# Performance work log

Measured on AMD Instinct MI355X. Metric: run time of the kernel, lower is better.

## Reference

```python
import jax, jax.numpy as jnp
import numpy as np

N_NODES = 50000
N_EDGES = 800000
DIMS = [128, 512, 256, 128]
EPS = 1e-5


def setup_inputs() -> dict:
    key = jax.random.key(0)
    ks = jax.random.split(key, 2 + 5 * 3)
    inp = {
        "x": jax.random.normal(ks[0], (N_NODES, DIMS[0]), dtype=jnp.float32),
        "edge_index": jax.random.randint(ks[1], (2, N_EDGES), 0, N_NODES, dtype=jnp.int64),
    }
    ki = 2
    for i in range(3):
        din, dout = DIMS[i], DIMS[i + 1]
        s = 1.0 / np.sqrt(din)
        inp[f"Wl{i}"] = jax.random.uniform(ks[ki + 0], (din, dout), jnp.float32, -s, s)
        inp[f"bl{i}"] = jax.random.uniform(ks[ki + 1], (dout,), jnp.float32, -s, s)
        inp[f"Wr{i}"] = jax.random.uniform(ks[ki + 2], (din, dout), jnp.float32, -s, s)
        inp[f"g{i}"] = jnp.ones((dout,), jnp.float32)
        inp[f"b{i}"] = jnp.zeros((dout,), jnp.float32)
        ki += 5
    return inp


def _sage_mean(x, src, dst, Wl, bl, Wr):
    n = x.shape[0]
    agg = jax.ops.segment_sum(x[src], dst, num_segments=n)  # [N, din]
    deg = jax.ops.segment_sum(jnp.ones((src.shape[0],), x.dtype), dst, num_segments=n)
    mean = agg / jnp.maximum(deg, 1.0)[:, None]
    return mean @ Wl + bl + x @ Wr


def _bn(h, gamma, beta):
    m = h.mean(axis=0)
    v = h.var(axis=0)
    return gamma * (h - m) * jax.lax.rsqrt(v + EPS) + beta


def reference(x, edge_index, Wl0, bl0, Wr0, g0, b0, Wl1, bl1, Wr1, g1, b1, Wl2, bl2, Wr2, g2, b2):
    src, dst = edge_index[0], edge_index[1]
    params = [(Wl0, bl0, Wr0, g0, b0), (Wl1, bl1, Wr1, g1, b1), (Wl2, bl2, Wr2, g2, b2)]
    h = x
    for Wl, bl, Wr, g, b in params:
        h = _sage_mean(h, src, dst, Wl, bl, Wr)
        h = _bn(h, g, b)
        h = jax.nn.relu(h)
        # dropout: identity in eval mode
    return h
```

## Files before the change

kernel.cpp:

```cpp
#include <hip/hip_runtime.h>
#include <cstdint>
#include <cstddef>


#define EPS_BN 1e-5f

typedef unsigned short ushort_t;
typedef __attribute__((ext_vector_type(8))) short short8;
typedef __attribute__((ext_vector_type(4))) float float4v;

__device__ __forceinline__ float bf2f(ushort_t u) {
    union { unsigned int i; float f; } v; v.i = ((unsigned int)u) << 16; return v.f;
}
__device__ __forceinline__ ushort_t f2bf(float f) {
    union { float f; unsigned int i; } v; v.f = f;
    unsigned int r = v.i + 0x7fffu + ((v.i >> 16) & 1u);
    return (ushort_t)(r >> 16);
}

__device__ __forceinline__ void async_copy16(void* lds, const void* g) {
    __builtin_amdgcn_global_load_lds(
        (const __attribute__((address_space(1))) unsigned int*)g,
        (__attribute__((address_space(3))) unsigned int*)lds, 16, 0, 0);
}

__global__ void detect_fmt_kernel(const int* __restrict__ edges, int* __restrict__ nz) {
    int t = threadIdx.x;
    int cnt = 0;
    #pragma unroll
    for (int j = 0; j < 4; ++j) {
        int idx = 2 * (t * 4 + j) + 1;
        if (edges[idx] != 0) cnt++;
    }
    if (cnt) atomicAdd(nz, cnt);
}

__device__ __forceinline__ void edge_sd(const int* __restrict__ p, int e, int ne,
                                        bool is64, int& s, int& d) {
    if (is64) { s = p[2 * e];  d = p[2 * ne + 2 * e]; }
    else      { s = p[e];      d = p[ne + e]; }
}
__device__ __forceinline__ int edge_d(const int* __restrict__ p, int e, int ne, bool is64) {
    return is64 ? p[2 * ne + 2 * e] : p[ne + e];
}

#define EPB 2048

__global__ __launch_bounds__(256) void bhist_kernel(
    const int* __restrict__ edges, int ne, const int* __restrict__ nz,
    int* __restrict__ gcnt) {
    __shared__ int h[256];
    int t = threadIdx.x;
    h[t] = 0;
    __syncthreads();
    bool is64 = (*nz == 0);
    int base_e = blockIdx.x * EPB;
    #pragma unroll
    for (int u = 0; u < EPB / 256; ++u) {
        int i = base_e + u * 256 + t;
        if (i < ne) atomicAdd(&h[edge_d(edges, i, ne, is64) >> 8], 1);
    }
    __syncthreads();
    if (h[t]) atomicAdd(&gcnt[t], h[t]);
}

__global__ __launch_bounds__(256) void bscan_kernel(
    const int* __restrict__ gcnt, int nb, int ne,
    int* __restrict__ bbase, int* __restrict__ bcur) {
    __shared__ int sh[256];
    int t = threadIdx.x;
    int v = (t < nb) ? gcnt[t] : 0;
    sh[t] = v;
    __syncthreads();
    for (int o = 1; o < 256; o <<= 1) {
        int x = (t >= o) ? sh[t - o] : 0;
        __syncthreads();
        sh[t] += x;
        __syncthreads();
    }
    int excl = sh[t] - v;
    if (t < nb) { bbase[t] = excl; bcur[t] = excl; }
    if (t == nb) bbase[t] = ne;
    if (nb == 256 && t == 0) {  }
    if (t == 0 && nb == 256) bbase[256] = ne;
}

__global__ __launch_bounds__(256) void bscatter_kernel(
    const int* __restrict__ edges, int ne, const int* __restrict__ nz,
    int* __restrict__ bcur, int* __restrict__ packed) {
    __shared__ int h[256];
    __shared__ int chunkb[256];
    __shared__ int lcur[256];
    int t = threadIdx.x;
    h[t] = 0;
    lcur[t] = 0;
    __syncthreads();
    bool is64 = (*nz == 0);
    int base_e = blockIdx.x * EPB;
    int ent[EPB / 256], eb[EPB / 256];
    #pragma unroll
    for (int u = 0; u < EPB / 256; ++u) {
        int i = base_e + u * 256 + t;
        if (i < ne) {
            int s, d;
            edge_sd(edges, i, ne, is64, s, d);
            ent[u] = s | ((d & 255) << 24);
            eb[u] = d >> 8;
            atomicAdd(&h[eb[u]], 1);
        } else eb[u] = -1;
    }
    __syncthreads();
    if (h[t]) chunkb[t] = atomicAdd(&bcur[t], h[t]);
    __syncthreads();
    #pragma unroll
    for (int u = 0; u < EPB / 256; ++u) {
        if (eb[u] >= 0) {
            int lp = atomicAdd(&lcur[eb[u]], 1);
            packed[chunkb[eb[u]] + lp] = ent[u];
        }
    }
}

__global__ __launch_bounds__(256) void bbuild_kernel(
    const int* __restrict__ packed, const int* __restrict__ bbase,
    int* __restrict__ rowptr, int* __restrict__ csr_src, int n) {
    __shared__ int h[256];
    __shared__ int cur[256];
    int t = threadIdx.x;
    int bb = blockIdx.x;
    int base = bbase[bb], cnt = bbase[bb + 1] - base;
    h[t] = 0;
    __syncthreads();
    for (int i = t; i < cnt; i += 256)
        atomicAdd(&h[(unsigned)packed[base + i] >> 24], 1);
    __syncthreads();
    int v = h[t];
    for (int o = 1; o < 256; o <<= 1) {
        int x = (t >= o) ? h[t - o] : 0;
        __syncthreads();
        h[t] += x;
        __syncthreads();
    }
    int excl = h[t] - v;
    int node = bb * 256 + t;
    if (node <= n) rowptr[node] = base + excl;
    cur[t] = excl;
    __syncthreads();
    for (int i = t; i < cnt; i += 256) {
        int e = packed[base + i];
        int lp = atomicAdd(&cur[(unsigned)e >> 24], 1);
        csr_src[base + lp] = e & 0xffffff;
    }
}

__global__ void f2b_kernel(const float* __restrict__ in, ushort_t* __restrict__ out, int n) {
    int i = blockIdx.x * 256 + threadIdx.x;
    if (i < n) out[i] = f2bf(in[i]);
}

__global__ void prep_wt_kernel(const float* __restrict__ Wl, const float* __restrict__ Wr,
                               ushort_t* __restrict__ WT, int K1, int Dout) {
    int idx = blockIdx.x * 256 + threadIdx.x;
    int K2 = 2 * K1;
    if (idx >= Dout * K2) return;
    int n = idx / K2, k = idx - n * K2;
    float v = (k < K1) ? Wl[(size_t)k * Dout + n] : Wr[(size_t)(k - K1) * Dout + n];
    WT[idx] = f2bf(v);
}

__global__ void prep_wtc_kernel(const float* __restrict__ Wl, const float* __restrict__ Wr,
                                ushort_t* __restrict__ WTc, int K, int D) {
    int idx = blockIdx.x * 256 + threadIdx.x;
    if (idx >= 2 * D * K) return;
    int nn = idx / K, k = idx - nn * K;
    float v = (nn < D) ? Wl[(size_t)k * D + nn] : Wr[(size_t)k * D + (nn - D)];
    WTc[idx] = f2bf(v);
}

template <int VEC> struct VecT;
template <> struct VecT<2> { using T = unsigned int; };
template <> struct VecT<4> { using T = uint2; };
template <> struct VecT<8> { using T = uint4; };

template <int VEC>
__device__ __forceinline__ void vunpack(typename VecT<VEC>::T v, unsigned int* w) {
    if constexpr (VEC == 2) { w[0] = v; }
    else if constexpr (VEC == 4) { w[0] = v.x; w[1] = v.y; }
    else { w[0] = v.x; w[1] = v.y; w[2] = v.z; w[3] = v.w; }
}

template <int VEC>
__device__ __forceinline__ void vaccum(typename VecT<VEC>::T v, float* acc) {
    unsigned int w[VEC / 2];
    vunpack<VEC>(v, w);
    #pragma unroll
    for (int i = 0; i < VEC / 2; ++i) {
        acc[2 * i + 0] += bf2f((ushort_t)(w[i] & 0xffffu));
        acc[2 * i + 1] += bf2f((ushort_t)(w[i] >> 16));
    }
}

template <int VEC>
__device__ __forceinline__ void gather_sum(
    const ushort_t* __restrict__ base, const int* __restrict__ csr_src,
    int e0, int e1, int rstride, float* acc) {
    using VT = typename VecT<VEC>::T;
    int e = e0;
    for (; e + 8 <= e1; e += 8) {
        VT v[8];
        #pragma unroll
        for (int u = 0; u < 8; ++u)
            v[u] = *(const VT*)(base + (size_t)csr_src[e + u] * rstride);
        #pragma unroll
        for (int u = 0; u < 8; ++u) vaccum<VEC>(v[u], acc);
    }
    if (e + 4 <= e1) {
        VT v[4];
        #pragma unroll
        for (int u = 0; u < 4; ++u)
            v[u] = *(const VT*)(base + (size_t)csr_src[e + u] * rstride);
        #pragma unroll
        for (int u = 0; u < 4; ++u) vaccum<VEC>(v[u], acc);
        e += 4;
    }
    if (e + 2 <= e1) {
        VT v0 = *(const VT*)(base + (size_t)csr_src[e] * rstride);
        VT v1 = *(const VT*)(base + (size_t)csr_src[e + 1] * rstride);
        vaccum<VEC>(v0, acc); vaccum<VEC>(v1, acc);
        e += 2;
    }
    if (e < e1)
        vaccum<VEC>(*(const VT*)(base + (size_t)csr_src[e] * rstride), acc);
}

template <int VEC>
__global__ __launch_bounds__(256) void aggregate_wave_kernel(
    const ushort_t* __restrict__ h, ushort_t* __restrict__ mean,
    const int* __restrict__ rowptr, const int* __restrict__ csr_src, int nnodes) {
    const int din = VEC * 64;
    int wid = blockIdx.x * 4 + (threadIdx.x >> 6);
    if (wid >= nnodes) return;
    int lane = threadIdx.x & 63;
    int e0 = rowptr[wid], e1 = rowptr[wid + 1];

    float acc[VEC];
    #pragma unroll
    for (int i = 0; i < VEC; ++i) acc[i] = 0.f;
    gather_sum<VEC>(h + (size_t)lane * VEC, csr_src, e0, e1, din, acc);

    int deg = e1 - e0;
    float scale = 1.0f / (float)(deg > 1 ? deg : 1);
    unsigned int o[VEC / 2];
    #pragma unroll
    for (int i = 0; i < VEC / 2; ++i)
        o[i] = (unsigned int)f2bf(acc[2 * i] * scale) |
               ((unsigned int)f2bf(acc[2 * i + 1] * scale) << 16);
    using VT = typename VecT<VEC>::T;
    VT ov;
    if constexpr (VEC == 2) { ov = o[0]; }
    else if constexpr (VEC == 4) { ov.x = o[0]; ov.y = o[1]; }
    else { ov.x = o[0]; ov.y = o[1]; ov.z = o[2]; ov.w = o[3]; }
    *(VT*)(mean + (size_t)wid * din + (size_t)lane * VEC) = ov;
}

template <int VEC>
__global__ __launch_bounds__(256) void aggregate_add_kernel(
    const ushort_t* __restrict__ PR, const float* __restrict__ bias,
    ushort_t* __restrict__ pre,
    const int* __restrict__ rowptr, const int* __restrict__ csr_src, int nnodes) {
    const int D = VEC * 64;
    const int stride = 2 * D;
    int wid = blockIdx.x * 4 + (threadIdx.x >> 6);
    if (wid >= nnodes) return;
    int lane = threadIdx.x & 63;
    int e0 = rowptr[wid], e1 = rowptr[wid + 1];

    float acc[VEC];
    #pragma unroll
    for (int i = 0; i < VEC; ++i) acc[i] = 0.f;
    gather_sum<VEC>(PR + (size_t)lane * VEC, csr_src, e0, e1, stride, acc);

    int deg = e1 - e0;
    float scale = 1.0f / (float)(deg > 1 ? deg : 1);

    using VT = typename VecT<VEC>::T;
    VT rv = *(const VT*)(PR + (size_t)wid * stride + D + (size_t)lane * VEC);
    unsigned int rw[VEC / 2];
    vunpack<VEC>(rv, rw);
    float o[VEC];
    #pragma unroll
    for (int i = 0; i < VEC / 2; ++i) {
        o[2 * i + 0] = bf2f((ushort_t)(rw[i] & 0xffffu));
        o[2 * i + 1] = bf2f((ushort_t)(rw[i] >> 16));
    }
    #pragma unroll
    for (int i = 0; i < VEC; ++i)
        o[i] += acc[i] * scale + bias[lane * VEC + i];

    unsigned int ow[VEC / 2];
    #pragma unroll
    for (int i = 0; i < VEC / 2; ++i)
        ow[i] = (unsigned int)f2bf(o[2 * i]) | ((unsigned int)f2bf(o[2 * i + 1]) << 16);
    VT ov;
    if constexpr (VEC == 2) { ov = ow[0]; }
    else if constexpr (VEC == 4) { ov.x = ow[0]; ov.y = ow[1]; }
    else { ov.x = ow[0]; ov.y = ow[1]; ov.z = ow[2]; ov.w = ow[3]; }
    *(VT*)(pre + (size_t)wid * D + (size_t)lane * VEC) = ov;
}

template <bool DUAL, bool BIAS>
__global__ __launch_bounds__(256) void gemm_glds_kernel(
    const ushort_t* __restrict__ A1, const ushort_t* __restrict__ A2,
    const ushort_t* __restrict__ BT, const float* __restrict__ bias,
    ushort_t* __restrict__ Cb, int N, int K1, int Ktot, int Wtot) {
    __shared__ ushort_t As[128 * 64];
    __shared__ ushort_t Bs[128 * 64];

    const int tid = threadIdx.x;
    const int wave = tid >> 6;
    const int lane = tid & 63;
    const int quad = lane >> 4;
    const int l15 = lane & 15;
    const int sw7 = l15 & 7;
    const int rowBase = blockIdx.y * 128;
    const int colBase = blockIdx.x * 128;
    const int wm = (wave >> 1) * 64;
    const int wn = (wave & 1) * 64;

    float4v acc[4][4];
    #pragma unroll
    for (int i = 0; i < 4; ++i)
        #pragma unroll
        for (int j = 0; j < 4; ++j)
            acc[i][j] = (float4v){0.f, 0.f, 0.f, 0.f};

    const int nkt = Ktot / 64;
    const int khalf = K1 / 64;

    for (int kt = 0; kt < nkt; ++kt) {
        const ushort_t* Asrc = A1;
        int kg = kt * 64;
        if (DUAL && kt >= khalf) { Asrc = A2; kg = (kt - khalf) * 64; }
        const int kb = kt * 64;

        #pragma unroll
        for (int u = 0; u < 4; ++u) {
            int c = u * 256 + tid;
            int r = c >> 3, cc = c & 7;
            int off = (cc ^ (r & 7)) * 8;
            int grow = rowBase + r;
            if (grow >= N) grow = N - 1;
            async_copy16(&As[c * 8], Asrc + (size_t)grow * K1 + kg + off);
            async_copy16(&Bs[c * 8], BT + (size_t)(colBase + r) * Ktot + kb + off);
        }
        __syncthreads();

        #pragma unroll
        for (int kh = 0; kh < 2; ++kh) {
            int cidx = kh * 4 + quad;
            short8 af[4], bf4[4];
            #pragma unroll
            for (int i = 0; i < 4; ++i)
                af[i] = *(const short8*)&As[(wm + i * 16 + l15) * 64 + (cidx ^ sw7) * 8];
            #pragma unroll
            for (int j = 0; j < 4; ++j)
                bf4[j] = *(const short8*)&Bs[(wn + j * 16 + l15) * 64 + (cidx ^ sw7) * 8];
            #pragma unroll
            for (int i = 0; i < 4; ++i)
                #pragma unroll
                for (int j = 0; j < 4; ++j)
                    acc[i][j] = __builtin_amdgcn_mfma_f32_16x16x32_bf16(bf4[j], af[i], acc[i][j], 0, 0, 0);
        }
        __syncthreads();
    }

    ushort_t* lws = &As[wave * 2048];
    #pragma unroll
    for (int p = 0; p < 2; ++p) {
        #pragma unroll
        for (int jj = 0; jj < 2; ++jj) {
            int j = 2 * p + jj;
            float4 bv = make_float4(0.f, 0.f, 0.f, 0.f);
            if (BIAS) bv = *(const float4*)(bias + colBase + wn + j * 16 + quad * 4);
            #pragma unroll
            for (int i = 0; i < 4; ++i) {
                uint2 pk;
                pk.x = (unsigned int)f2bf(acc[i][j][0] + bv.x) |
                       ((unsigned int)f2bf(acc[i][j][1] + bv.y) << 16);
                pk.y = (unsigned int)f2bf(acc[i][j][2] + bv.z) |
                       ((unsigned int)f2bf(acc[i][j][3] + bv.w) << 16);
                *(uint2*)&lws[(i * 16 + l15) * 32 + jj * 16 + quad * 4] = pk;
            }
        }
        __syncthreads();
        #pragma unroll
        for (int it = 0; it < 4; ++it) {
            int c = it * 64 + lane;
            int row = c >> 2, coff = (c & 3) * 8;
            int grow = rowBase + wm + row;
            if (grow < N) {
                uint4 v = *(const uint4*)&lws[row * 32 + coff];
                *(uint4*)(Cb + (size_t)grow * Wtot + colBase + wn + p * 32 + coff) = v;
            }
        }
        __syncthreads();
    }
}

__global__ void colstats_b_kernel(const ushort_t* __restrict__ h, int N, int D,
                                  float* __restrict__ sum, float* __restrict__ sumsq) {
    int c2 = blockIdx.x * 128 + (threadIdx.x & 63) * 2;
    int rl = threadIdx.x >> 6;
    float s0 = 0.f, s20 = 0.f, s1 = 0.f, s21 = 0.f;
    int stride = gridDim.y * 4;
    for (int r = blockIdx.y * 4 + rl; r < N; r += stride) {
        unsigned int w = *(const unsigned int*)(h + (size_t)r * D + c2);
        float v0 = bf2f((ushort_t)(w & 0xffffu));
        float v1 = bf2f((ushort_t)(w >> 16));
        s0 += v0; s20 += v0 * v0;
        s1 += v1; s21 += v1 * v1;
    }
    atomicAdd(&sum[c2 + 0], s0);
    atomicAdd(&sumsq[c2 + 0], s20);
    atomicAdd(&sum[c2 + 1], s1);
    atomicAdd(&sumsq[c2 + 1], s21);
}

__global__ void bn_relu_b2b_kernel(const ushort_t* __restrict__ h, ushort_t* __restrict__ hb,
                                   int N, int D,
                                   const float* __restrict__ sum, const float* __restrict__ sumsq,
                                   const float* __restrict__ g, const float* __restrict__ b) {
    size_t idx = (size_t)blockIdx.x * blockDim.x + threadIdx.x;
    size_t tot = (size_t)N * D / 2;
    if (idx >= tot) return;
    int cp = (int)(idx & (size_t)(D / 2 - 1));
    int c0 = cp * 2, c1 = c0 + 1;
    float m0 = sum[c0] / (float)N, m1 = sum[c1] / (float)N;
    float i0 = rsqrtf(sumsq[c0] / (float)N - m0 * m0 + EPS_BN);
    float i1 = rsqrtf(sumsq[c1] / (float)N - m1 * m1 + EPS_BN);
    unsigned int w = ((const unsigned int*)h)[idx];
    float v0 = g[c0] * (bf2f((ushort_t)(w & 0xffffu)) - m0) * i0 + b[c0];
    float v1 = g[c1] * (bf2f((ushort_t)(w >> 16)) - m1) * i1 + b[c1];
    v0 = v0 > 0.f ? v0 : 0.f;
    v1 = v1 > 0.f ? v1 : 0.f;
    ((unsigned int*)hb)[idx] = (unsigned int)f2bf(v0) | ((unsigned int)f2bf(v1) << 16);
}

__global__ void bn_relu_b2f_kernel(const ushort_t* __restrict__ h, float* __restrict__ hf,
                                   int N, int D,
                                   const float* __restrict__ sum, const float* __restrict__ sumsq,
                                   const float* __restrict__ g, const float* __restrict__ b) {
    size_t idx = (size_t)blockIdx.x * blockDim.x + threadIdx.x;
    size_t tot = (size_t)N * D / 2;
    if (idx >= tot) return;
    int cp = (int)(idx & (size_t)(D / 2 - 1));
    int c0 = cp * 2, c1 = c0 + 1;
    float m0 = sum[c0] / (float)N, m1 = sum[c1] / (float)N;
    float i0 = rsqrtf(sumsq[c0] / (float)N - m0 * m0 + EPS_BN);
    float i1 = rsqrtf(sumsq[c1] / (float)N - m1 * m1 + EPS_BN);
    unsigned int w = ((const unsigned int*)h)[idx];
    float v0 = g[c0] * (bf2f((ushort_t)(w & 0xffffu)) - m0) * i0 + b[c0];
    float v1 = g[c1] * (bf2f((ushort_t)(w >> 16)) - m1) * i1 + b[c1];
    float2 o;
    o.x = v0 > 0.f ? v0 : 0.f;
    o.y = v1 > 0.f ? v1 : 0.f;
    *(float2*)(hf + idx * 2) = o;
}

extern "C" void kernel_launch(void* const* d_in, const int* in_sizes, int n_in,
                              void* d_out, int out_size, void* d_ws, size_t ws_size,
                              hipStream_t stream) {
    const float* x     = (const float*)d_in[0];
    const int*   edges = (const int*)d_in[1];
    const float* Wl0 = (const float*)d_in[2];
    const float* bl0 = (const float*)d_in[3];
    const float* Wr0 = (const float*)d_in[4];
    const float* g0  = (const float*)d_in[5];
    const float* b0  = (const float*)d_in[6];
    const float* Wl1 = (const float*)d_in[7];
    const float* bl1 = (const float*)d_in[8];
    const float* Wr1 = (const float*)d_in[9];
    const float* g1  = (const float*)d_in[10];
    const float* b1  = (const float*)d_in[11];
    const float* Wl2 = (const float*)d_in[12];
    const float* bl2 = (const float*)d_in[13];
    const float* Wr2 = (const float*)d_in[14];
    const float* g2  = (const float*)d_in[15];
    const float* b2  = (const float*)d_in[16];

    const int D0 = 128, D1 = 512, D2 = 256, D3 = 128;
    const int n  = in_sizes[0] / D0;
    const int ne = in_sizes[1] / 2;
    const int NB = (n + 255) >> 8;

    char* base = (char*)d_ws;
    size_t off = 0;
    auto alloc = [&](size_t bytes) -> char* {
        char* p = base + off;
        off = (off + bytes + 255) & ~(size_t)255;
        return p;
    };
    int*      nzflag  = (int*)alloc(4);
    int*      gcnt    = (int*)alloc(256 * 4);
    float*    stats   = (float*)alloc(6 * 512 * 4);
    size_t    zero_span = off;
    int*      bbase   = (int*)alloc(257 * 4);
    int*      bcur    = (int*)alloc(256 * 4);
    int*      packed  = (int*)alloc((size_t)ne * 4);
    int*      rowptr  = (int*)alloc((size_t)(n + 1) * 4);
    int*      csr_src = (int*)alloc((size_t)ne * 4);
    ushort_t* xb      = (ushort_t*)alloc((size_t)n * D0 * 2);
    ushort_t* mb      = (ushort_t*)alloc((size_t)n * 512 * 2);
    ushort_t* h1b     = (ushort_t*)alloc((size_t)n * D1 * 2);
    ushort_t* h2b     = (ushort_t*)alloc((size_t)n * D2 * 2);
    ushort_t* hpre    = (ushort_t*)alloc((size_t)n * 512 * 2);
    ushort_t* WT0     = (ushort_t*)alloc((size_t)D1 * 2 * D0 * 2);
    ushort_t* WT1c    = (ushort_t*)alloc((size_t)(2 * D2) * D1 * 2);
    ushort_t* WT2c    = (ushort_t*)alloc((size_t)(2 * D3) * D2 * 2);
    float*    out     = (float*)d_out;
    (void)ws_size; (void)n_in; (void)out_size;

    hipMemsetAsync(base, 0, zero_span, stream);

    detect_fmt_kernel<<<1, 256, 0, stream>>>(edges, nzflag);
    int ablk = (ne + EPB - 1) / EPB;
    bhist_kernel<<<ablk, 256, 0, stream>>>(edges, ne, nzflag, gcnt);
    bscan_kernel<<<1, 256, 0, stream>>>(gcnt, NB, ne, bbase, bcur);
    bscatter_kernel<<<ablk, 256, 0, stream>>>(edges, ne, nzflag, bcur, packed);
    bbuild_kernel<<<NB, 256, 0, stream>>>(packed, bbase, rowptr, csr_src, n);

    f2b_kernel<<<((size_t)n * D0 + 255) / 256, 256, 0, stream>>>(x, xb, n * D0);
    prep_wt_kernel<<<(D1 * 2 * D0 + 255) / 256, 256, 0, stream>>>(Wl0, Wr0, WT0, D0, D1);
    prep_wtc_kernel<<<(2 * D2 * D1 + 255) / 256, 256, 0, stream>>>(Wl1, Wr1, WT1c, D1, D2);
    prep_wtc_kernel<<<(2 * D3 * D2 + 255) / 256, 256, 0, stream>>>(Wl2, Wr2, WT2c, D2, D3);

    const int aggGrid = (n + 3) / 4;
    const int rowBlocks = (n + 127) / 128;
    float* st0 = stats + 0 * 1024;
    float* st1 = stats + 1 * 1024;
    float* st2 = stats + 2 * 1024;

    aggregate_wave_kernel<2><<<aggGrid, 256, 0, stream>>>(xb, mb, rowptr, csr_src, n);
    gemm_glds_kernel<true, true><<<dim3(D1 / 128, rowBlocks), 256, 0, stream>>>(
        mb, xb, WT0, bl0, hpre, n, D0, 2 * D0, D1);
    colstats_b_kernel<<<dim3(D1 / 128, 128), 256, 0, stream>>>(hpre, n, D1, st0, st0 + 512);
    bn_relu_b2b_kernel<<<((size_t)n * D1 / 2 + 255) / 256, 256, 0, stream>>>(
        hpre, h1b, n, D1, st0, st0 + 512, g0, b0);

    gemm_glds_kernel<false, false><<<dim3(2 * D2 / 128, rowBlocks), 256, 0, stream>>>(
        h1b, nullptr, WT1c, nullptr, mb, n, D1, D1, 2 * D2);
    aggregate_add_kernel<4><<<aggGrid, 256, 0, stream>>>(
        mb, bl1, hpre, rowptr, csr_src, n);
    colstats_b_kernel<<<dim3(D2 / 128, 128), 256, 0, stream>>>(hpre, n, D2, st1, st1 + 512);
    bn_relu_b2b_kernel<<<((size_t)n * D2 / 2 + 255) / 256, 256, 0, stream>>>(
        hpre, h2b, n, D2, st1, st1 + 512, g1, b1);

    gemm_glds_kernel<false, false><<<dim3(2 * D3 / 128, rowBlocks), 256, 0, stream>>>(
        h2b, nullptr, WT2c, nullptr, mb, n, D2, D2, 2 * D3);
    aggregate_add_kernel<2><<<aggGrid, 256, 0, stream>>>(
        mb, bl2, hpre, rowptr, csr_src, n);
    colstats_b_kernel<<<dim3(D3 / 128, 128), 256, 0, stream>>>(hpre, n, D3, st2, st2 + 512);
    bn_relu_b2f_kernel<<<((size_t)n * D3 / 2 + 255) / 256, 256, 0, stream>>>(
        hpre, out, n, D3, st2, st2 + 512, g2, b2);
}
```

Measured before the change: 596.7 us.

## Slice feature columns across blocks in neighbor aggregation kernels

Replaces the one-wave-per-node aggregation kernels with a sliced kernel. Each 16-lane group handles one node and 32 bf16 columns, and the feature width is split across several blocks. The intent is for concurrently running blocks to share a column slice so gathered rows stay in L2/cache, and to expose more parallelism with narrower per-lane loads. It also simplifies bf16 unpacking with mask/shift helpers. The cost is that every edge index is reread once per slice, and loads become 4-byte scalar gathers.

```diff
diff --git a/kernel.cpp b/kernel.cpp
--- a/kernel.cpp
+++ b/kernel.cpp
@@ -11,6 +11,12 @@
 
 __device__ __forceinline__ float bf2f(ushort_t u) {
     union { unsigned int i; float f; } v; v.i = ((unsigned int)u) << 16; return v.f;
+}
+__device__ __forceinline__ float bflo(unsigned int w) {
+    union { unsigned int i; float f; } v; v.i = w << 16; return v.f;
+}
+__device__ __forceinline__ float bfhi(unsigned int w) {
+    union { unsigned int i; float f; } v; v.i = w & 0xffff0000u; return v.f;
 }
 __device__ __forceinline__ ushort_t f2bf(float f) {
     union { float f; unsigned int i; } v; v.f = f;
@@ -81,7 +87,6 @@
     int excl = sh[t] - v;
     if (t < nb) { bbase[t] = excl; bcur[t] = excl; }
     if (t == nb) bbase[t] = ne;
-    if (nb == 256 && t == 0) {  }
     if (t == 0 && nb == 256) bbase[256] = ne;
 }
 
@@ -177,135 +182,64 @@
     WTc[idx] = f2bf(v);
 }
 
-template <int VEC> struct VecT;
-template <> struct VecT<2> { using T = unsigned int; };
-template <> struct VecT<4> { using T = uint2; };
-template <> struct VecT<8> { using T = uint4; };
-
-template <int VEC>
-__device__ __forceinline__ void vunpack(typename VecT<VEC>::T v, unsigned int* w) {
-    if constexpr (VEC == 2) { w[0] = v; }
-    else if constexpr (VEC == 4) { w[0] = v.x; w[1] = v.y; }
-    else { w[0] = v.x; w[1] = v.y; w[2] = v.z; w[3] = v.w; }
-}
-
-template <int VEC>
-__device__ __forceinline__ void vaccum(typename VecT<VEC>::T v, float* acc) {
-    unsigned int w[VEC / 2];
-    vunpack<VEC>(v, w);
-    #pragma unroll
-    for (int i = 0; i < VEC / 2; ++i) {
-        acc[2 * i + 0] += bf2f((ushort_t)(w[i] & 0xffffu));
-        acc[2 * i + 1] += bf2f((ushort_t)(w[i] >> 16));
-    }
-}
-
-template <int VEC>
-__device__ __forceinline__ void gather_sum(
-    const ushort_t* __restrict__ base, const int* __restrict__ csr_src,
-    int e0, int e1, int rstride, float* acc) {
-    using VT = typename VecT<VEC>::T;
+template <bool ADD>
+__global__ __launch_bounds__(256) void aggregate_sliced_kernel(
+    const ushort_t* __restrict__ srcm, const float* __restrict__ bias,
+    ushort_t* __restrict__ outb,
+    const int* __restrict__ rowptr, const int* __restrict__ csr_src,
+    int nnodes, int nsl, int rstride_u, int outw_u) {
+    int slice = blockIdx.x % nsl;
+    int nb = blockIdx.x / nsl;
+    int g = threadIdx.x >> 4;
+    int lg = threadIdx.x & 15;
+    int node = nb * 16 + g;
+    if (node >= nnodes) return;
+    int e0 = rowptr[node], e1 = rowptr[node + 1];
+
+    const unsigned int* base = (const unsigned int*)srcm + (size_t)slice * 16 + lg;
+    float a0 = 0.f, a1 = 0.f;
     int e = e0;
     for (; e + 8 <= e1; e += 8) {
-        VT v[8];
+        unsigned int w[8];
         #pragma unroll
         for (int u = 0; u < 8; ++u)
-            v[u] = *(const VT*)(base + (size_t)csr_src[e + u] * rstride);
-        #pragma unroll
-        for (int u = 0; u < 8; ++u) vaccum<VEC>(v[u], acc);
+            w[u] = base[(size_t)csr_src[e + u] * rstride_u];
+        #pragma unroll
+        for (int u = 0; u < 8; ++u) { a0 += bflo(w[u]); a1 += bfhi(w[u]); }
     }
     if (e + 4 <= e1) {
-        VT v[4];
+        unsigned int w[4];
         #pragma unroll
         for (int u = 0; u < 4; ++u)
-            v[u] = *(const VT*)(base + (size_t)csr_src[e + u] * rstride);
-        #pragma unroll
-        for (int u = 0; u < 4; ++u) vaccum<VEC>(v[u], acc);
+            w[u] = base[(size_t)csr_src[e + u] * rstride_u];
+        #pragma unroll
+        for (int u = 0; u < 4; ++u) { a0 += bflo(w[u]); a1 += bfhi(w[u]); }
         e += 4;
     }
     if (e + 2 <= e1) {
-        VT v0 = *(const VT*)(base + (size_t)csr_src[e] * rstride);
-        VT v1 = *(const VT*)(base + (size_t)csr_src[e + 1] * rstride);
-        vaccum<VEC>(v0, acc); vaccum<VEC>(v1, acc);
+        unsigned int w0 = base[(size_t)csr_src[e] * rstride_u];
+        unsigned int w1 = base[(size_t)csr_src[e + 1] * rstride_u];
+        a0 += bflo(w0) + bflo(w1);
+        a1 += bfhi(w0) + bfhi(w1);
         e += 2;
     }
-    if (e < e1)
-        vaccum<VEC>(*(const VT*)(base + (size_t)csr_src[e] * rstride), acc);
-}
-
-template <int VEC>
-__global__ __launch_bounds__(256) void aggregate_wave_kernel(
-    const ushort_t* __restrict__ h, ushort_t* __restrict__ mean,
-    const int* __restrict__ rowptr, const int* __restrict__ csr_src, int nnodes) {
-    const int din = VEC * 64;
-    int wid = blockIdx.x * 4 + (threadIdx.x >> 6);
-    if (wid >= nnodes) return;
-    int lane = threadIdx.x & 63;
-    int e0 = rowptr[wid], e1 = rowptr[wid + 1];
-
-    float acc[VEC];
-    #pragma unroll
-    for (int i = 0; i < VEC; ++i) acc[i] = 0.f;
-    gather_sum<VEC>(h + (size_t)lane * VEC, csr_src, e0, e1, din, acc);
+    if (e < e1) {
+        unsigned int w0 = base[(size_t)csr_src[e] * rstride_u];
+        a0 += bflo(w0); a1 += bfhi(w0);
+    }
 
     int deg = e1 - e0;
     float scale = 1.0f / (float)(deg > 1 ? deg : 1);
-    unsigned int o[VEC / 2];
-    #pragma unroll
-    for (int i = 0; i < VEC / 2; ++i)
-        o[i] = (unsigned int)f2bf(acc[2 * i] * scale) |
-               ((unsigned int)f2bf(acc[2 * i + 1] * scale) << 16);
-    using VT = typename VecT<VEC>::T;
-    VT ov;
-    if constexpr (VEC == 2) { ov = o[0]; }
-    else if constexpr (VEC == 4) { ov.x = o[0]; ov.y = o[1]; }
-    else { ov.x = o[0]; ov.y = o[1]; ov.z = o[2]; ov.w = o[3]; }
-    *(VT*)(mean + (size_t)wid * din + (size_t)lane * VEC) = ov;
-}
-
-template <int VEC>
-__global__ __launch_bounds__(256) void aggregate_add_kernel(
-    const ushort_t* __restrict__ PR, const float* __restrict__ bias,
-    ushort_t* __restrict__ pre,
-    const int* __restrict__ rowptr, const int* __restrict__ csr_src, int nnodes) {
-    const int D = VEC * 64;
-    const int stride = 2 * D;
-    int wid = blockIdx.x * 4 + (threadIdx.x >> 6);
-    if (wid >= nnodes) return;
-    int lane = threadIdx.x & 63;
-    int e0 = rowptr[wid], e1 = rowptr[wid + 1];
-
-    float acc[VEC];
-    #pragma unroll
-    for (int i = 0; i < VEC; ++i) acc[i] = 0.f;
-    gather_sum<VEC>(PR + (size_t)lane * VEC, csr_src, e0, e1, stride, acc);
-
-    int deg = e1 - e0;
-    float scale = 1.0f / (float)(deg > 1 ? deg : 1);
-
-    using VT = typename VecT<VEC>::T;
-    VT rv = *(const VT*)(PR + (size_t)wid * stride + D + (size_t)lane * VEC);
-    unsigned int rw[VEC / 2];
-    vunpack<VEC>(rv, rw);
-    float o[VEC];
-    #pragma unroll
-    for (int i = 0; i < VEC / 2; ++i) {
-        o[2 * i + 0] = bf2f((ushort_t)(rw[i] & 0xffffu));
-        o[2 * i + 1] = bf2f((ushort_t)(rw[i] >> 16));
-    }
-    #pragma unroll
-    for (int i = 0; i < VEC; ++i)
-        o[i] += acc[i] * scale + bias[lane * VEC + i];
-
-    unsigned int ow[VEC / 2];
-    #pragma unroll
-    for (int i = 0; i < VEC / 2; ++i)
-        ow[i] = (unsigned int)f2bf(o[2 * i]) | ((unsigned int)f2bf(o[2 * i + 1]) << 16);
-    VT ov;
-    if constexpr (VEC == 2) { ov = ow[0]; }
-    else if constexpr (VEC == 4) { ov.x = ow[0]; ov.y = ow[1]; }
-    else { ov.x = ow[0]; ov.y = ow[1]; ov.z = ow[2]; ov.w = ow[3]; }
-    *(VT*)(pre + (size_t)wid * D + (size_t)lane * VEC) = ov;
+    float o0 = a0 * scale, o1 = a1 * scale;
+    if (ADD) {
+        unsigned int rw = ((const unsigned int*)srcm)
+            [(size_t)node * rstride_u + outw_u + slice * 16 + lg];
+        float2 bv = *(const float2*)(bias + slice * 32 + lg * 2);
+        o0 += bflo(rw) + bv.x;
+        o1 += bfhi(rw) + bv.y;
+    }
+    ((unsigned int*)outb)[(size_t)node * outw_u + slice * 16 + lg] =
+        (unsigned int)f2bf(o0) | ((unsigned int)f2bf(o1) << 16);
 }
 
 template <bool DUAL, bool BIAS>
@@ -415,8 +349,7 @@
     int stride = gridDim.y * 4;
     for (int r = blockIdx.y * 4 + rl; r < N; r += stride) {
         unsigned int w = *(const unsigned int*)(h + (size_t)r * D + c2);
-        float v0 = bf2f((ushort_t)(w & 0xffffu));
-        float v1 = bf2f((ushort_t)(w >> 16));
+        float v0 = bflo(w), v1 = bfhi(w);
         s0 += v0; s20 += v0 * v0;
         s1 += v1; s21 += v1 * v1;
     }
@@ -439,8 +372,8 @@
     float i0 = rsqrtf(sumsq[c0] / (float)N - m0 * m0 + EPS_BN);
     float i1 = rsqrtf(sumsq[c1] / (float)N - m1 * m1 + EPS_BN);
     unsigned int w = ((const unsigned int*)h)[idx];
-    float v0 = g[c0] * (bf2f((ushort_t)(w & 0xffffu)) - m0) * i0 + b[c0];
-    float v1 = g[c1] * (bf2f((ushort_t)(w >> 16)) - m1) * i1 + b[c1];
+    float v0 = g[c0] * (bflo(w) - m0) * i0 + b[c0];
+    float v1 = g[c1] * (bfhi(w) - m1) * i1 + b[c1];
     v0 = v0 > 0.f ? v0 : 0.f;
     v1 = v1 > 0.f ? v1 : 0.f;
     ((unsigned int*)hb)[idx] = (unsigned int)f2bf(v0) | ((unsigned int)f2bf(v1) << 16);
@@ -459,8 +392,8 @@
     float i0 = rsqrtf(sumsq[c0] / (float)N - m0 * m0 + EPS_BN);
     float i1 = rsqrtf(sumsq[c1] / (float)N - m1 * m1 + EPS_BN);
     unsigned int w = ((const unsigned int*)h)[idx];
-    float v0 = g[c0] * (bf2f((ushort_t)(w & 0xffffu)) - m0) * i0 + b[c0];
-    float v1 = g[c1] * (bf2f((ushort_t)(w >> 16)) - m1) * i1 + b[c1];
+    float v0 = g[c0] * (bflo(w) - m0) * i0 + b[c0];
+    float v1 = g[c1] * (bfhi(w) - m1) * i1 + b[c1];
     float2 o;
     o.x = v0 > 0.f ? v0 : 0.f;
     o.y = v1 > 0.f ? v1 : 0.f;
@@ -534,13 +467,14 @@
     prep_wtc_kernel<<<(2 * D2 * D1 + 255) / 256, 256, 0, stream>>>(Wl1, Wr1, WT1c, D1, D2);
     prep_wtc_kernel<<<(2 * D3 * D2 + 255) / 256, 256, 0, stream>>>(Wl2, Wr2, WT2c, D2, D3);
 
-    const int aggGrid = (n + 3) / 4;
     const int rowBlocks = (n + 127) / 128;
+    const int nodeBlocks = (n + 15) / 16;
     float* st0 = stats + 0 * 1024;
     float* st1 = stats + 1 * 1024;
     float* st2 = stats + 2 * 1024;
 
-    aggregate_wave_kernel<2><<<aggGrid, 256, 0, stream>>>(xb, mb, rowptr, csr_src, n);
+    aggregate_sliced_kernel<false><<<4 * nodeBlocks, 256, 0, stream>>>(
+        xb, nullptr, mb, rowptr, csr_src, n, 4, D0 / 2, D0 / 2);
     gemm_glds_kernel<true, true><<<dim3(D1 / 128, rowBlocks), 256, 0, stream>>>(
         mb, xb, WT0, bl0, hpre, n, D0, 2 * D0, D1);
     colstats_b_kernel<<<dim3(D1 / 128, 128), 256, 0, stream>>>(hpre, n, D1, st0, st0 + 512);
@@ -549,16 +483,16 @@
 
     gemm_glds_kernel<false, false><<<dim3(2 * D2 / 128, rowBlocks), 256, 0, stream>>>(
         h1b, nullptr, WT1c, nullptr, mb, n, D1, D1, 2 * D2);
-    aggregate_add_kernel<4><<<aggGrid, 256, 0, stream>>>(
-        mb, bl1, hpre, rowptr, csr_src, n);
+    aggregate_sliced_kernel<true><<<8 * nodeBlocks, 256, 0, stream>>>(
+        mb, bl1, hpre, rowptr, csr_src, n, 8, D2, D2 / 2);
     colstats_b_kernel<<<dim3(D2 / 128, 128), 256, 0, stream>>>(hpre, n, D2, st1, st1 + 512);
     bn_relu_b2b_kernel<<<((size_t)n * D2 / 2 + 255) / 256, 256, 0, stream>>>(
         hpre, h2b, n, D2, st1, st1 + 512, g1, b1);
 
     gemm_glds_kernel<false, false><<<dim3(2 * D3 / 128, rowBlocks), 256, 0, stream>>>(
         h2b, nullptr, WT2c, nullptr, mb, n, D2, D2, 2 * D3);
-    aggregate_add_kernel<2><<<aggGrid, 256, 0, stream>>>(
-        mb, bl2, hpre, rowptr, csr_src, n);
+    aggregate_sliced_kernel<true><<<4 * nodeBlocks, 256, 0, stream>>>(
+        mb, bl2, hpre, rowptr, csr_src, n, 4, D3, D3 / 2);
     colstats_b_kernel<<<dim3(D3 / 128, 128), 256, 0, stream>>>(hpre, n, D3, st2, st2 + 512);
     bn_relu_b2f_kernel<<<((size_t)n * D3 / 2 + 255) / 256, 256, 0, stream>>>(
         hpre, out, n, D3, st2, st2 + 512, g2, b2);
```

Measured after the change: 653.3 us. 1.09x slower.
